# Kernel optimization log

Hardware: AMD Instinct MI355X
Metric: run time of the kernel (lower is better)

## Reference

```python
import jax, jax.numpy as jnp
import numpy as np

M = 4        # multi_anchor
B = 256      # graphs per batch
NPG = 64     # nodes per graph
N = B * NPG  # total nodes
DEG = 8
E = N * DEG
DF = 16      # raw node feature dim
D = 256      # emb_dim
L = 5        # num_layer
NA = 2       # num_anchor
TASKS = 10
T = 1.0


def _gnn_node(h, edge_src, edge_dst, gin_W1, gin_b1, gin_W2, gin_b2, eps):
    # GIN-style message passing: gather -> sum-scatter -> 2-layer MLP, per layer.
    for l in range(L):
        msg = h[:, edge_src]                                  # [M,E,D] gather
        agg = jnp.zeros_like(h).at[:, edge_dst].add(msg)      # [M,N,D] scatter-add
        z = (1.0 + eps[l]) * h + agg
        z = jax.nn.relu(z @ gin_W1[l] + gin_b1[l])
        h = jax.nn.relu(z @ gin_W2[l] + gin_b2[l])
    return h


def _mindist(h):
    # per-node min squared distance to other nodes in the same graph
    hg = h.reshape(M, B, NPG, D)
    sq = jnp.sum(hg * hg, axis=-1)                            # [M,B,n]
    d2 = sq[..., :, None] + sq[..., None, :] - 2.0 * jnp.einsum('mbid,mbjd->mbij', hg, hg)
    d2 = jnp.maximum(d2, 0.0) + jnp.eye(NPG, dtype=h.dtype) * 1e9
    return jnp.min(d2, axis=-1).reshape(M, N)


def reference(x, W_enc, b_enc, gin_W1, gin_b1, gin_W2, gin_b2, eps,
              anchor_emb, W_n2n, b_n2n, W_pred, b_pred, edge_src, edge_dst):
    # InputEncoder (float x -> MLP with tail activation)
    h0 = jax.nn.relu(x @ W_enc + b_enc)                       # [N,D]
    tx = jnp.broadcast_to(h0[None], (M, N, D))                # expand over multi_anchor
    anchor = jnp.zeros((M, N), dtype=jnp.int32)
    xcur = tx
    skey = jax.random.key(42)
    goff = jnp.arange(B) * NPG                                # graph offsets
    rows = jnp.arange(M)[:, None]
    for i in range(1, NA + 1):
        h = _gnn_node(xcur, edge_src, edge_dst, gin_W1, gin_b1, gin_W2, gin_b2, eps)
        mind = _mindist(h)                                    # [M,N]
        pred = -mind - 10.0 * (anchor > 0).astype(h.dtype)    # mask prior anchors
        logits = (pred * T).reshape(M, B, NPG)
        # categorical sample per (anchor-row, graph) via Gumbel-max == multinomial_sample_batch
        u = jax.random.uniform(jax.random.fold_in(skey, i), (M, B, NPG), minval=1e-9, maxval=1.0)
        idx = jnp.argmax(logits - jnp.log(-jnp.log(u)), axis=-1)  # [M,B]
        glob = idx + goff[None, :]
        anchor = anchor.at[rows, glob].set(i)
        xcur = tx * anchor_emb[anchor] + tx
    h = _gnn_node(xcur, edge_src, edge_dst, gin_W1, gin_b1, gin_W2, gin_b2, eps)
    hn = jax.nn.relu(h @ W_n2n + b_n2n)                       # node2node (tailact)
    hg = hn.reshape(M, B, NPG, D).mean(axis=2)                # mean graph pooling
    out = hg @ W_pred + b_pred                                # pred_lin
    return out.mean(axis=0)                                   # mean over multi_anchor -> [B,TASKS]


def setup_inputs():
    key = jax.random.key(0)
    ks = jax.random.split(key, 12)
    x = jax.random.normal(ks[0], (N, DF), dtype=jnp.float32)
    gid = jnp.repeat(jnp.arange(B), NPG * DEG)
    edge_src = gid * NPG + jax.random.randint(ks[1], (E,), 0, NPG)
    edge_dst = gid * NPG + jax.random.randint(ks[2], (E,), 0, NPG)
    s = lambda k, shp: (jax.random.normal(k, shp, dtype=jnp.float32) * 0.05)
    return {
        'x': x,
        'W_enc': s(ks[3], (DF, D)), 'b_enc': jnp.zeros((D,), jnp.float32),
        'gin_W1': s(ks[4], (L, D, D)), 'gin_b1': jnp.zeros((L, D), jnp.float32),
        'gin_W2': s(ks[5], (L, D, D)), 'gin_b2': jnp.zeros((L, D), jnp.float32),
        'eps': jnp.zeros((L,), jnp.float32),
        'anchor_emb': s(ks[6], (NA + 1, D)),
        'W_n2n': s(ks[7], (D, D)), 'b_n2n': jnp.zeros((D,), jnp.float32),
        'W_pred': s(ks[8], (D, TASKS)), 'b_pred': jnp.zeros((TASKS,), jnp.float32),
        'edge_src': edge_src, 'edge_dst': edge_dst,
    }
```

## Files before the change

kernel.cpp:

```cpp
#include <hip/hip_runtime.h>
#include <stdint.h>

typedef unsigned short u16;
typedef _Float16 f16;
typedef f16 f16x8 __attribute__((ext_vector_type(8)));
typedef float f32x16 __attribute__((ext_vector_type(16)));

#define M_     4
#define B_     256
#define NPG_   64
#define N_     (B_*NPG_)
#define DEG_   8
#define E_     (N_*DEG_)
#define DF_    16
#define D_     256
#define L_     5
#define NA_    2
#define TASKS_ 10

#define HROW 520
#define MFMA16(a,b,c) __builtin_amdgcn_mfma_f32_32x32x16_f16(a,b,c,0,0,0)

__device__ __forceinline__ u16 h_bits(f16 h) { union { f16 h; u16 u; } c; c.h = h; return c.u; }
__device__ __forceinline__ f16 bits_h(u16 u) { union { u16 u; f16 h; } c; c.u = u; return c.h; }
__device__ __forceinline__ float h2f(u16 u) { return (float)bits_h(u); }
__device__ __forceinline__ void split_f16(float v, u16& hi, u16& lo) {
  f16 h = (f16)v;
  f16 l = (f16)(v - (float)h);
  hi = h_bits(h); lo = h_bits(l);
}

__device__ __forceinline__ int haddr8(int row, int chunk) {
  return row * HROW + ((chunk ^ (row & 7)) << 4);
}
__device__ __forceinline__ void write_split(u16* hfU, int row, int col, float v) {
  const int ad = haddr8(row, col >> 3) + (col & 7);
  u16 hi, lo; split_f16(v, hi, lo);
  hfU[ad] = hi; hfU[ad + 8] = lo;
}
__device__ __forceinline__ void write_hi(u16* hfU, int row, int col, float v) {
  const int ad = haddr8(row, col >> 3) + (col & 7);
  hfU[ad] = h_bits((f16)v);
}

__device__ __forceinline__ uint32_t rotl32(uint32_t v, int r) { return (v << r) | (v >> (32 - r)); }
__device__ __forceinline__ void threefry2x32(uint32_t k0, uint32_t k1, uint32_t x0, uint32_t x1,
                                             uint32_t& o0, uint32_t& o1) {
  const uint32_t ks2 = k0 ^ k1 ^ 0x1BD11BDAu;
  x0 += k0; x1 += k1;
#define TFR(r) { x0 += x1; x1 = rotl32(x1, r); x1 ^= x0; }
  TFR(13) TFR(15) TFR(26) TFR(6)   x0 += k1;  x1 += ks2 + 1u;
  TFR(17) TFR(29) TFR(16) TFR(24)  x0 += ks2; x1 += k0 + 2u;
  TFR(13) TFR(15) TFR(26) TFR(6)   x0 += k0;  x1 += k1 + 3u;
  TFR(17) TFR(29) TFR(16) TFR(24)  x0 += k1;  x1 += ks2 + 4u;
  TFR(13) TFR(15) TFR(26) TFR(6)   x0 += ks2; x1 += k0 + 5u;
#undef TFR
  o0 = x0; o1 = x1;
}

template<int TERMS>
__device__ __forceinline__ void gemm_w_mfma(u16* __restrict__ hfU, const u16* __restrict__ WTm,
                                            const float* __restrict__ bias, bool do_relu) {
  const int tid = threadIdx.x;
  const int lane = tid & 63, w = tid >> 6;
  const int l31 = lane & 31, lh = lane >> 5;
  const int col = w * 32 + l31;
  const float bv = bias[col];

  f32x16 acc0 = {}, acc1 = {};
  const u16* Bbase = WTm + col * 8;
#pragma unroll
  for (int ks = 0; ks < 16; ++ks) {
    const int chunk = ks * 2 + lh;
    const int a0 = haddr8(l31, chunk);
    const int a1 = haddr8(32 + l31, chunk);
    const f16x8 ahi0 = *(const f16x8*)(hfU + a0);
    const f16x8 ahi1 = *(const f16x8*)(hfU + a1);
    const f16x8 bh = *(const f16x8*)(Bbase + chunk * 2048);
    if (TERMS == 3) {
      const f16x8 alo0 = *(const f16x8*)(hfU + a0 + 8);
      const f16x8 alo1 = *(const f16x8*)(hfU + a1 + 8);
      const f16x8 bl = *(const f16x8*)(Bbase + chunk * 2048 + 65536);
      acc0 = MFMA16(ahi0, bh, acc0);
      acc0 = MFMA16(ahi0, bl, acc0);
      acc0 = MFMA16(alo0, bh, acc0);
      acc1 = MFMA16(ahi1, bh, acc1);
      acc1 = MFMA16(ahi1, bl, acc1);
      acc1 = MFMA16(alo1, bh, acc1);
    } else {
      acc0 = MFMA16(ahi0, bh, acc0);
      acc1 = MFMA16(ahi1, bh, acc1);
    }
  }
  __syncthreads();
#pragma unroll
  for (int r = 0; r < 16; ++r) {
    const int rr = (r & 3) + 8 * (r >> 2) + 4 * lh;
    float v0 = acc0[r] + bv;
    float v1 = acc1[r] + bv;
    if (do_relu) { v0 = fmaxf(v0, 0.f); v1 = fmaxf(v1, 0.f); }
    if (TERMS == 3) {
      write_split(hfU, rr, col, v0);
      write_split(hfU, 32 + rr, col, v1);
    } else {
      write_hi(hfU, rr, col, v0);
      write_hi(hfU, 32 + rr, col, v1);
    }
  }
  __syncthreads();
}

template<int TERMS>
__device__ __forceinline__ void gemm_adj_mfma(u16* __restrict__ hfU, const u16* __restrict__ AdjU,
                                              float epsl) {
  const int tid = threadIdx.x;
  const int lane = tid & 63, w = tid >> 6;
  const int l31 = lane & 31, lh = lane >> 5;
  const int d = w * 32 + l31;
  const int dc = d >> 3, de = d & 7;
  f32x16 acc0 = {}, acc1 = {};
#pragma unroll
  for (int kk = 0; kk < 4; ++kk) {
    const f16x8 A0 = *(const f16x8*)(AdjU + l31 * 72 + (kk * 2 + lh) * 8);
    const f16x8 A1 = *(const f16x8*)(AdjU + (32 + l31) * 72 + (kk * 2 + lh) * 8);
    const int jb = kk * 16 + lh * 8;
    f16x8 bh, bl;
#pragma unroll
    for (int jj = 0; jj < 8; ++jj) {
      const int j = jb + jj;
      const int ad = haddr8(j, dc) + de;
      bh[jj] = bits_h(hfU[ad]);
      if (TERMS == 3) bl[jj] = bits_h(hfU[ad + 8]);
    }
    acc0 = MFMA16(A0, bh, acc0);
    acc1 = MFMA16(A1, bh, acc1);
    if (TERMS == 3) {
      acc0 = MFMA16(A0, bl, acc0);
      acc1 = MFMA16(A1, bl, acc1);
    }
  }
  float self0[16], self1[16];
#pragma unroll
  for (int r = 0; r < 16; ++r) {
    const int rr = (r & 3) + 8 * (r >> 2) + 4 * lh;
    { const int ad = haddr8(rr, dc) + de;
      self0[r] = (TERMS == 3) ? (h2f(hfU[ad]) + h2f(hfU[ad + 8])) : h2f(hfU[ad]); }
    { const int ad = haddr8(32 + rr, dc) + de;
      self1[r] = (TERMS == 3) ? (h2f(hfU[ad]) + h2f(hfU[ad + 8])) : h2f(hfU[ad]); }
  }
  __syncthreads();
#pragma unroll
  for (int r = 0; r < 16; ++r) {
    const int rr = (r & 3) + 8 * (r >> 2) + 4 * lh;
    if (TERMS == 3) {
      write_split(hfU, rr, d, acc0[r] + epsl * self0[r]);
      write_split(hfU, 32 + rr, d, acc1[r] + epsl * self1[r]);
    } else {
      write_hi(hfU, rr, d, acc0[r] + epsl * self0[r]);
      write_hi(hfU, 32 + rr, d, acc1[r] + epsl * self1[r]);
    }
  }
  __syncthreads();
}

__device__ __forceinline__ void mindist_mfma(u16* __restrict__ hfU, float* __restrict__ mindS) {
  const int tid = threadIdx.x;
  const int lane = tid & 63, w = tid >> 6;
  const int gb = w & 3, gi = gb >> 1, gj = gb & 1, ks = w >> 2;
  const int l31 = lane & 31, lh = lane >> 5;
  f32x16 acc = {};
#pragma unroll
  for (int t = 0; t < 8; ++t) {
    const int chunk = 4 * t + 2 * ks + lh;
    const int ra = haddr8(gi * 32 + l31, chunk);
    const int rb_ = haddr8(gj * 32 + l31, chunk);
    const f16x8 ahi = *(const f16x8*)(hfU + ra);
    const f16x8 alo = *(const f16x8*)(hfU + ra + 8);
    const f16x8 bhi = *(const f16x8*)(hfU + rb_);
    const f16x8 blo = *(const f16x8*)(hfU + rb_ + 8);
    acc = MFMA16(ahi, bhi, acc);
    acc = MFMA16(ahi, blo, acc);
    acc = MFMA16(alo, bhi, acc);
  }
  __syncthreads();
  float* hfF = (float*)hfU;
  if (ks == 1) {
#pragma unroll
    for (int r = 0; r < 16; ++r) {
      const int rr = (r & 3) + 8 * (r >> 2) + 4 * lh;
      hfF[gb * 1088 + rr * 34 + l31] = acc[r];
    }
  }
  __syncthreads();
  if (ks == 0) {
#pragma unroll
    for (int r = 0; r < 16; ++r) {
      const int rr = (r & 3) + 8 * (r >> 2) + 4 * lh;
      const float g = acc[r] + hfF[gb * 1088 + rr * 34 + l31];
      hfF[8192 + (gi * 32 + rr) * 66 + gj * 32 + l31] = g;
    }
  }
  __syncthreads();
  {
    const int i = tid >> 3, jt = tid & 7;
    const float gii = hfF[8192 + i * 66 + i];
    float dmin = 3.4e38f;
#pragma unroll
    for (int jj = 0; jj < 8; ++jj) {
      const int j = jt * 8 + jj;
      const float gjj = hfF[8192 + j * 66 + j];
      const float gij = hfF[8192 + i * 66 + j];
      float d2 = fmaxf(gii + gjj - 2.f * gij, 0.f);
      if (j == i) d2 += 1e9f;
      dmin = fminf(dmin, d2);
    }
    dmin = fminf(dmin, __shfl_xor(dmin, 1));
    dmin = fminf(dmin, __shfl_xor(dmin, 2));
    dmin = fminf(dmin, __shfl_xor(dmin, 4));
    if (jt == 0) mindS[i] = dmin;
  }
  __syncthreads();
}

__device__ __forceinline__ void stage_adj(u16* AdjU, const float* AdjF, int b, int tid) {
  const float* src = AdjF + b * 4096;
  for (int t = tid; t < 4096; t += 512)
    AdjU[(t >> 6) * 72 + (t & 63)] = h_bits((f16)src[t]);
}

template<bool WRITE_LO>
__device__ __forceinline__ void build_xcur(u16* hfU, const float* h0g, const float* aemb,
                                           const int* anchorS, int b, int tid) {
  const int i = tid >> 3, part = tid & 7;
  const float* t = h0g + (b * 64 + i) * 256;
  const float* e = aemb + anchorS[i] * D_;
#pragma unroll
  for (int c = 0; c < 4; ++c) {
    const int chunk = part * 4 + c;
    const float4 tv0 = *(const float4*)(t + chunk * 8);
    const float4 tv1 = *(const float4*)(t + chunk * 8 + 4);
    const float4 ev0 = *(const float4*)(e + chunk * 8);
    const float4 ev1 = *(const float4*)(e + chunk * 8 + 4);
    float vv[8];
    vv[0] = fmaf(tv0.x, ev0.x, tv0.x); vv[1] = fmaf(tv0.y, ev0.y, tv0.y);
    vv[2] = fmaf(tv0.z, ev0.z, tv0.z); vv[3] = fmaf(tv0.w, ev0.w, tv0.w);
    vv[4] = fmaf(tv1.x, ev1.x, tv1.x); vv[5] = fmaf(tv1.y, ev1.y, tv1.y);
    vv[6] = fmaf(tv1.z, ev1.z, tv1.z); vv[7] = fmaf(tv1.w, ev1.w, tv1.w);
    f16x8 hi8, lo8;
#pragma unroll
    for (int ee = 0; ee < 8; ++ee) { u16 h, l; split_f16(vv[ee], h, l); hi8[ee] = bits_h(h); lo8[ee] = bits_h(l); }
    const int a = haddr8(i, chunk);
    *(f16x8*)(hfU + a) = hi8;
    if (WRITE_LO) *(f16x8*)(hfU + a + 8) = lo8;
  }
}

__device__ __forceinline__ void sample_anchor(const float* mindS, float* scoreS, int* anchorS,
                                              int m, int b, int iter, int tid) {
  if (tid < 64) {
    const int j = tid;
    uint32_t k0, k1;
    threefry2x32(0u, 42u, 0u, (uint32_t)iter, k0, k1);
    const uint32_t p = (uint32_t)(m * (B_ * NPG_) + b * NPG_ + j);
    uint32_t o0, o1, bits;
    if (p < 32768u) { threefry2x32(k0, k1, p, p + 32768u, o0, o1); bits = o0; }
    else            { threefry2x32(k0, k1, p - 32768u, p, o0, o1); bits = o1; }
    const float f = __uint_as_float((bits >> 9) | 0x3f800000u) - 1.0f;
    const float uv = fmaxf(1e-9f, f + 1e-9f);
    const float pred = -mindS[j] - ((anchorS[j] > 0) ? 10.0f : 0.0f);
    scoreS[j] = pred - logf(-logf(uv));
  }
  __syncthreads();
  if (tid == 0) {
    int best = 0; float bv = scoreS[0];
    for (int j = 1; j < 64; ++j) { const float v = scoreS[j]; if (v > bv) { bv = v; best = j; } }
    anchorS[best] = iter;
  }
}

__global__ void build_adj_kernel(const int* __restrict__ esrc, const int* __restrict__ edst,
                                 float* __restrict__ AdjF) {
  const int e = blockIdx.x * 256 + threadIdx.x;
  if (e < E_) {
    const int s = esrc[e];
    const int d = edst[e];
    const int g = s >> 6;
    atomicAdd(AdjF + g * 4096 + (d & 63) * 64 + (s & 63), 1.0f);
  }
}

__global__ __launch_bounds__(256) void prep_wt(const float* __restrict__ gW1, const float* __restrict__ gW2,
                                               const float* __restrict__ Wn2n, u16* __restrict__ WTbuf) {
  const int mat = blockIdx.x;
  const float* Wsrc = (mat < 5) ? (gW1 + mat * 65536)
                    : (mat < 10) ? (gW2 + (mat - 5) * 65536) : Wn2n;
  u16* dst = WTbuf + (size_t)mat * 131072;
  const int base = blockIdx.y * 2048;
  for (int idx = base + threadIdx.x; idx < base + 2048; idx += 256) {
    const int k = idx >> 8, d = idx & 255;
    const float a = Wsrc[idx];
    u16 hi, lo; split_f16(a, hi, lo);
    const int off = (k >> 3) * 2048 + d * 8 + (k & 7);
    dst[off] = hi;
    dst[65536 + off] = lo;
  }
}

__global__ __launch_bounds__(512)
void gnn1_kernel(const float* __restrict__ x, const float* __restrict__ Wenc,
                 const float* __restrict__ benc, float* __restrict__ h0g,
                 const float* __restrict__ AdjF, const u16* __restrict__ WTbuf,
                 const float* __restrict__ gb1, const float* __restrict__ gb2,
                 const float* __restrict__ eps, float* __restrict__ mindG) {
  __shared__ __align__(16) u16 hfU[64 * HROW];
  __shared__ __align__(16) u16 AdjU[64 * 72];
  __shared__ float mindS[64];
  const int tid = threadIdx.x;
  const int b = blockIdx.x;

  {
    float* scr = (float*)hfU;
    for (int t = tid; t < 4096; t += 512) {
      const int k = t >> 8, d = t & 255;
      scr[k * 264 + d + (d >> 5)] = Wenc[t];
    }
    if (tid < 256) scr[4300 + tid] = benc[tid];
    for (int t = tid; t < 1024; t += 512) scr[4600 + t] = x[b * 1024 + t];
    __syncthreads();

    const int i = tid >> 3, part = tid & 7;
    float xv[16];
#pragma unroll
    for (int k = 0; k < 16; ++k) xv[k] = scr[4600 + i * 16 + k];
    float hv[32];
#pragma unroll
    for (int dd = 0; dd < 32; ++dd) {
      const int d = part * 32 + dd;
      float acc = scr[4300 + d];
#pragma unroll
      for (int k = 0; k < 16; ++k) acc = fmaf(xv[k], scr[k * 264 + d + (d >> 5)], acc);
      hv[dd] = fmaxf(acc, 0.f);
    }
    float* dst = h0g + (b * 64 + i) * 256 + part * 32;
#pragma unroll
    for (int dd = 0; dd < 32; dd += 4) {
      float4 v; v.x = hv[dd]; v.y = hv[dd + 1]; v.z = hv[dd + 2]; v.w = hv[dd + 3];
      *(float4*)(dst + dd) = v;
    }
    __syncthreads();
#pragma unroll
    for (int c = 0; c < 4; ++c) {
      f16x8 hi8, lo8;
#pragma unroll
      for (int e = 0; e < 8; ++e) { u16 h, l; split_f16(hv[c * 8 + e], h, l); hi8[e] = bits_h(h); lo8[e] = bits_h(l); }
      const int a = haddr8(i, part * 4 + c);
      *(f16x8*)(hfU + a) = hi8;
      *(f16x8*)(hfU + a + 8) = lo8;
    }
  }
  stage_adj(AdjU, AdjF, b, tid);
  __syncthreads();

  for (int l = 0; l < L_; ++l) {
    const float epsl = 1.0f + eps[l];
    gemm_adj_mfma<3>(hfU, AdjU, epsl);
    gemm_w_mfma<3>(hfU, WTbuf + (size_t)l * 131072,       gb1 + l * D_, true);
    gemm_w_mfma<3>(hfU, WTbuf + (size_t)(5 + l) * 131072, gb2 + l * D_, true);
  }
  mindist_mfma(hfU, mindS);
  if (tid < 64) mindG[b * 64 + tid] = mindS[tid];
}

__global__ __launch_bounds__(512, 4)
void mega_kernel(const float* __restrict__ h0g, const float* __restrict__ AdjF,
                 const u16* __restrict__ WTbuf,
                 const float* __restrict__ gb1, const float* __restrict__ gb2,
                 const float* __restrict__ eps, const float* __restrict__ aemb,
                 const float* __restrict__ bn2n,
                 const float* __restrict__ Wpred, const float* __restrict__ bpred,
                 const float* __restrict__ mindG, float* __restrict__ outp) {
  __shared__ __align__(16) u16 hfU[64 * HROW];
  __shared__ __align__(16) u16 AdjU[64 * 72];
  __shared__ float mindS[64];
  __shared__ float scoreS[64];
  __shared__ float hgS[256];
  __shared__ int   anchorS[64];

  const int tid = threadIdx.x;
  const int b = blockIdx.x;
  const int m = blockIdx.y;

  stage_adj(AdjU, AdjF, b, tid);
  if (tid < 64) { anchorS[tid] = 0; mindS[tid] = mindG[b * 64 + tid]; }
  __syncthreads();

  sample_anchor(mindS, scoreS, anchorS, m, b, 1, tid);
  __syncthreads();
  build_xcur<true>(hfU, h0g, aemb, anchorS, b, tid);
  __syncthreads();

  for (int l = 0; l < L_; ++l) {
    const float epsl = 1.0f + eps[l];
    gemm_adj_mfma<3>(hfU, AdjU, epsl);
    gemm_w_mfma<3>(hfU, WTbuf + (size_t)l * 131072,       gb1 + l * D_, true);
    gemm_w_mfma<3>(hfU, WTbuf + (size_t)(5 + l) * 131072, gb2 + l * D_, true);
  }
  mindist_mfma(hfU, mindS);
  sample_anchor(mindS, scoreS, anchorS, m, b, 2, tid);
  __syncthreads();
  build_xcur<false>(hfU, h0g, aemb, anchorS, b, tid);
  __syncthreads();

  for (int l = 0; l < L_; ++l) {
    const float epsl = 1.0f + eps[l];
    gemm_adj_mfma<1>(hfU, AdjU, epsl);
    gemm_w_mfma<1>(hfU, WTbuf + (size_t)l * 131072,       gb1 + l * D_, true);
    gemm_w_mfma<1>(hfU, WTbuf + (size_t)(5 + l) * 131072, gb2 + l * D_, true);
  }

  gemm_w_mfma<1>(hfU, WTbuf + (size_t)10 * 131072, bn2n, true);
  if (tid < 256) {
    const int dc = tid >> 3, de = tid & 7;
    float s = 0.f;
    for (int i = 0; i < 64; ++i)
      s += h2f(hfU[haddr8(i, dc) + de]);
    hgS[tid] = s * (1.0f / 64.0f);
  }
  __syncthreads();
  if (tid < 160) {
    const int t = tid >> 4, part = tid & 15;
    float s = 0.f;
    for (int d = part * 16; d < part * 16 + 16; ++d) s = fmaf(hgS[d], Wpred[d * TASKS_ + t], s);
    s += __shfl_xor(s, 1); s += __shfl_xor(s, 2); s += __shfl_xor(s, 4); s += __shfl_xor(s, 8);
    if (part == 0) {
      float val = s * 0.25f;
      if (m == 0) val += bpred[t];
      atomicAdd(outp + b * TASKS_ + t, val);
    }
  }
}

extern "C" void kernel_launch(void* const* d_in, const int* in_sizes, int n_in,
                              void* d_out, int out_size, void* d_ws, size_t ws_size,
                              hipStream_t stream) {
  const float* x     = (const float*)d_in[0];
  const float* Wenc  = (const float*)d_in[1];
  const float* benc  = (const float*)d_in[2];
  const float* gW1   = (const float*)d_in[3];
  const float* gb1   = (const float*)d_in[4];
  const float* gW2   = (const float*)d_in[5];
  const float* gb2   = (const float*)d_in[6];
  const float* eps   = (const float*)d_in[7];
  const float* aemb  = (const float*)d_in[8];
  const float* Wn2n  = (const float*)d_in[9];
  const float* bn2n  = (const float*)d_in[10];
  const float* Wpred = (const float*)d_in[11];
  const float* bpred = (const float*)d_in[12];
  const int* esrc    = (const int*)d_in[13];
  const int* edst    = (const int*)d_in[14];
  float* outp = (float*)d_out;

  float* h0g  = (float*)d_ws;
  float* AdjF = h0g + (size_t)N_ * D_;
  u16* WTbuf  = (u16*)(AdjF + B_ * 4096);
  float* mindG = (float*)(WTbuf + (size_t)11 * 131072);

  hipMemsetAsync(AdjF, 0, (size_t)B_ * 4096 * sizeof(float), stream);
  hipMemsetAsync(outp, 0, (size_t)out_size * sizeof(float), stream);
  build_adj_kernel<<<dim3((E_ + 255) / 256), dim3(256), 0, stream>>>(esrc, edst, AdjF);
  prep_wt<<<dim3(11, 32), dim3(256), 0, stream>>>(gW1, gW2, Wn2n, WTbuf);
  gnn1_kernel<<<dim3(B_), dim3(512), 0, stream>>>(x, Wenc, benc, h0g, AdjF, WTbuf,
                                                  gb1, gb2, eps, mindG);
  mega_kernel<<<dim3(B_, M_), dim3(512), 0, stream>>>(h0g, AdjF, WTbuf, gb1, gb2,
                                                      eps, aemb, bn2n, Wpred, bpred, mindG, outp);
}
```

Before: 673.4 us.

## Split-K 1024-thread first GNN pass and ping-pong buffers in light GNN

The first-iteration GNN kernel (one block per graph, only 256 blocks) moves to 1024 threads, and its weight GEMMs are split along K across two wave groups with an LDS reduction. This raises per-block parallelism on a grid too small to fill the GPU. The low-precision second pass now ping-pongs between the hi and lo halves of the shared buffer, which lets each stage drop one barrier between reading and writing. Costs are extra LDS reduction traffic and barriers in the split-K path, plus idle waves in the adjacency and mindist stages.

After: 699.8 us. 1.04x slower.

```diff
diff --git a/kernel.cpp b/kernel.cpp
--- a/kernel.cpp
+++ b/kernel.cpp
@@ -37,10 +37,6 @@
   const int ad = haddr8(row, col >> 3) + (col & 7);
   u16 hi, lo; split_f16(v, hi, lo);
   hfU[ad] = hi; hfU[ad + 8] = lo;
-}
-__device__ __forceinline__ void write_hi(u16* hfU, int row, int col, float v) {
-  const int ad = haddr8(row, col >> 3) + (col & 7);
-  hfU[ad] = h_bits((f16)v);
 }
 
 __device__ __forceinline__ uint32_t rotl32(uint32_t v, int r) { return (v << r) | (v >> (32 - r)); }
@@ -58,8 +54,7 @@
   o0 = x0; o1 = x1;
 }
 
-template<int TERMS>
-__device__ __forceinline__ void gemm_w_mfma(u16* __restrict__ hfU, const u16* __restrict__ WTm,
+__device__ __forceinline__ void gemm_w_full(u16* __restrict__ hfU, const u16* __restrict__ WTm,
                                             const float* __restrict__ bias, bool do_relu) {
   const int tid = threadIdx.x;
   const int lane = tid & 63, w = tid >> 6;
@@ -76,21 +71,16 @@
     const int a1 = haddr8(32 + l31, chunk);
     const f16x8 ahi0 = *(const f16x8*)(hfU + a0);
     const f16x8 ahi1 = *(const f16x8*)(hfU + a1);
+    const f16x8 alo0 = *(const f16x8*)(hfU + a0 + 8);
+    const f16x8 alo1 = *(const f16x8*)(hfU + a1 + 8);
     const f16x8 bh = *(const f16x8*)(Bbase + chunk * 2048);
-    if (TERMS == 3) {
-      const f16x8 alo0 = *(const f16x8*)(hfU + a0 + 8);
-      const f16x8 alo1 = *(const f16x8*)(hfU + a1 + 8);
-      const f16x8 bl = *(const f16x8*)(Bbase + chunk * 2048 + 65536);
-      acc0 = MFMA16(ahi0, bh, acc0);
-      acc0 = MFMA16(ahi0, bl, acc0);
-      acc0 = MFMA16(alo0, bh, acc0);
-      acc1 = MFMA16(ahi1, bh, acc1);
-      acc1 = MFMA16(ahi1, bl, acc1);
-      acc1 = MFMA16(alo1, bh, acc1);
-    } else {
-      acc0 = MFMA16(ahi0, bh, acc0);
-      acc1 = MFMA16(ahi1, bh, acc1);
-    }
+    const f16x8 bl = *(const f16x8*)(Bbase + chunk * 2048 + 65536);
+    acc0 = MFMA16(ahi0, bh, acc0);
+    acc0 = MFMA16(ahi0, bl, acc0);
+    acc0 = MFMA16(alo0, bh, acc0);
+    acc1 = MFMA16(ahi1, bh, acc1);
+    acc1 = MFMA16(ahi1, bl, acc1);
+    acc1 = MFMA16(alo1, bh, acc1);
   }
   __syncthreads();
 #pragma unroll
@@ -99,19 +89,13 @@
     float v0 = acc0[r] + bv;
     float v1 = acc1[r] + bv;
     if (do_relu) { v0 = fmaxf(v0, 0.f); v1 = fmaxf(v1, 0.f); }
-    if (TERMS == 3) {
-      write_split(hfU, rr, col, v0);
-      write_split(hfU, 32 + rr, col, v1);
-    } else {
-      write_hi(hfU, rr, col, v0);
-      write_hi(hfU, 32 + rr, col, v1);
-    }
-  }
-  __syncthreads();
-}
-
-template<int TERMS>
-__device__ __forceinline__ void gemm_adj_mfma(u16* __restrict__ hfU, const u16* __restrict__ AdjU,
+    write_split(hfU, rr, col, v0);
+    write_split(hfU, 32 + rr, col, v1);
+  }
+  __syncthreads();
+}
+
+__device__ __forceinline__ void gemm_adj_full(u16* __restrict__ hfU, const u16* __restrict__ AdjU,
                                               float epsl) {
   const int tid = threadIdx.x;
   const int lane = tid & 63, w = tid >> 6;
@@ -127,38 +111,28 @@
     f16x8 bh, bl;
 #pragma unroll
     for (int jj = 0; jj < 8; ++jj) {
-      const int j = jb + jj;
-      const int ad = haddr8(j, dc) + de;
+      const int ad = haddr8(jb + jj, dc) + de;
       bh[jj] = bits_h(hfU[ad]);
-      if (TERMS == 3) bl[jj] = bits_h(hfU[ad + 8]);
+      bl[jj] = bits_h(hfU[ad + 8]);
     }
     acc0 = MFMA16(A0, bh, acc0);
     acc1 = MFMA16(A1, bh, acc1);
-    if (TERMS == 3) {
-      acc0 = MFMA16(A0, bl, acc0);
-      acc1 = MFMA16(A1, bl, acc1);
-    }
+    acc0 = MFMA16(A0, bl, acc0);
+    acc1 = MFMA16(A1, bl, acc1);
   }
   float self0[16], self1[16];
 #pragma unroll
   for (int r = 0; r < 16; ++r) {
     const int rr = (r & 3) + 8 * (r >> 2) + 4 * lh;
-    { const int ad = haddr8(rr, dc) + de;
-      self0[r] = (TERMS == 3) ? (h2f(hfU[ad]) + h2f(hfU[ad + 8])) : h2f(hfU[ad]); }
-    { const int ad = haddr8(32 + rr, dc) + de;
-      self1[r] = (TERMS == 3) ? (h2f(hfU[ad]) + h2f(hfU[ad + 8])) : h2f(hfU[ad]); }
+    { const int ad = haddr8(rr, dc) + de;      self0[r] = h2f(hfU[ad]) + h2f(hfU[ad + 8]); }
+    { const int ad = haddr8(32 + rr, dc) + de; self1[r] = h2f(hfU[ad]) + h2f(hfU[ad + 8]); }
   }
   __syncthreads();
 #pragma unroll
   for (int r = 0; r < 16; ++r) {
     const int rr = (r & 3) + 8 * (r >> 2) + 4 * lh;
-    if (TERMS == 3) {
-      write_split(hfU, rr, d, acc0[r] + epsl * self0[r]);
-      write_split(hfU, 32 + rr, d, acc1[r] + epsl * self1[r]);
-    } else {
-      write_hi(hfU, rr, d, acc0[r] + epsl * self0[r]);
-      write_hi(hfU, 32 + rr, d, acc1[r] + epsl * self1[r]);
-    }
+    write_split(hfU, rr, d, acc0[r] + epsl * self0[r]);
+    write_split(hfU, 32 + rr, d, acc1[r] + epsl * self1[r]);
   }
   __syncthreads();
 }
@@ -222,9 +196,244 @@
   __syncthreads();
 }
 
-__device__ __forceinline__ void stage_adj(u16* AdjU, const float* AdjF, int b, int tid) {
+__device__ __forceinline__ void gemm_w_light(u16* __restrict__ hfU, const u16* __restrict__ WTm,
+                                             const float* __restrict__ bias, bool do_relu,
+                                             int pin, int pout) {
+  const int tid = threadIdx.x;
+  const int lane = tid & 63, w = tid >> 6;
+  const int l31 = lane & 31, lh = lane >> 5;
+  const int col = w * 32 + l31;
+  const float bv = bias[col];
+  f32x16 acc0 = {}, acc1 = {};
+  const u16* Bbase = WTm + col * 8;
+#pragma unroll
+  for (int ks = 0; ks < 16; ++ks) {
+    const int chunk = ks * 2 + lh;
+    const f16x8 a0 = *(const f16x8*)(hfU + haddr8(l31, chunk) + pin);
+    const f16x8 a1 = *(const f16x8*)(hfU + haddr8(32 + l31, chunk) + pin);
+    const f16x8 bh = *(const f16x8*)(Bbase + chunk * 2048);
+    acc0 = MFMA16(a0, bh, acc0);
+    acc1 = MFMA16(a1, bh, acc1);
+  }
+#pragma unroll
+  for (int r = 0; r < 16; ++r) {
+    const int rr = (r & 3) + 8 * (r >> 2) + 4 * lh;
+    float v0 = acc0[r] + bv, v1 = acc1[r] + bv;
+    if (do_relu) { v0 = fmaxf(v0, 0.f); v1 = fmaxf(v1, 0.f); }
+    hfU[haddr8(rr, col >> 3) + (col & 7) + pout] = h_bits((f16)v0);
+    hfU[haddr8(32 + rr, col >> 3) + (col & 7) + pout] = h_bits((f16)v1);
+  }
+  __syncthreads();
+}
+
+__device__ __forceinline__ void gemm_adj_light(u16* __restrict__ hfU, const u16* __restrict__ AdjU,
+                                               float epsl, int pin, int pout) {
+  const int tid = threadIdx.x;
+  const int lane = tid & 63, w = tid >> 6;
+  const int l31 = lane & 31, lh = lane >> 5;
+  const int d = w * 32 + l31;
+  const int dc = d >> 3, de = d & 7;
+  f32x16 acc0 = {}, acc1 = {};
+#pragma unroll
+  for (int kk = 0; kk < 4; ++kk) {
+    const f16x8 A0 = *(const f16x8*)(AdjU + l31 * 72 + (kk * 2 + lh) * 8);
+    const f16x8 A1 = *(const f16x8*)(AdjU + (32 + l31) * 72 + (kk * 2 + lh) * 8);
+    const int jb = kk * 16 + lh * 8;
+    f16x8 bh;
+#pragma unroll
+    for (int jj = 0; jj < 8; ++jj)
+      bh[jj] = bits_h(hfU[haddr8(jb + jj, dc) + de + pin]);
+    acc0 = MFMA16(A0, bh, acc0);
+    acc1 = MFMA16(A1, bh, acc1);
+  }
+#pragma unroll
+  for (int r = 0; r < 16; ++r) {
+    const int rr = (r & 3) + 8 * (r >> 2) + 4 * lh;
+    const float s0 = h2f(hfU[haddr8(rr, dc) + de + pin]);
+    const float s1 = h2f(hfU[haddr8(32 + rr, dc) + de + pin]);
+    hfU[haddr8(rr, dc) + de + pout]      = h_bits((f16)(acc0[r] + epsl * s0));
+    hfU[haddr8(32 + rr, dc) + de + pout] = h_bits((f16)(acc1[r] + epsl * s1));
+  }
+  __syncthreads();
+}
+
+__device__ __forceinline__ void gemm_w3_ks1024(u16* __restrict__ hfU, const u16* __restrict__ WTm,
+                                               const float* __restrict__ bias, bool do_relu) {
+  const int tid = threadIdx.x;
+  const int lane = tid & 63, w = tid >> 6;
+  const int l31 = lane & 31, lh = lane >> 5;
+  const int ks = w >> 3;
+  const int cb = w & 7;
+  const int col = cb * 32 + l31;
+  const float bv = bias[col];
+
+  f32x16 acc0 = {}, acc1 = {};
+  const u16* Bbase = WTm + col * 8;
+#pragma unroll
+  for (int q = 0; q < 8; ++q) {
+    const int chunk = ks * 16 + q * 2 + lh;
+    const int a0 = haddr8(l31, chunk);
+    const int a1 = haddr8(32 + l31, chunk);
+    const f16x8 ahi0 = *(const f16x8*)(hfU + a0);
+    const f16x8 ahi1 = *(const f16x8*)(hfU + a1);
+    const f16x8 alo0 = *(const f16x8*)(hfU + a0 + 8);
+    const f16x8 alo1 = *(const f16x8*)(hfU + a1 + 8);
+    const f16x8 bh = *(const f16x8*)(Bbase + chunk * 2048);
+    const f16x8 bl = *(const f16x8*)(Bbase + chunk * 2048 + 65536);
+    acc0 = MFMA16(ahi0, bh, acc0);
+    acc0 = MFMA16(ahi0, bl, acc0);
+    acc0 = MFMA16(alo0, bh, acc0);
+    acc1 = MFMA16(ahi1, bh, acc1);
+    acc1 = MFMA16(ahi1, bl, acc1);
+    acc1 = MFMA16(alo1, bh, acc1);
+  }
+  __syncthreads();
+  float* scr = (float*)hfU;
+  if (ks == 1) {
+#pragma unroll
+    for (int r = 0; r < 16; ++r) {
+      const int rr = (r & 3) + 8 * (r >> 2) + 4 * lh;
+      scr[(cb * 64 + rr) * 32 + l31]      = acc0[r];
+      scr[(cb * 64 + 32 + rr) * 32 + l31] = acc1[r];
+    }
+  }
+  __syncthreads();
+  float sc0[16], sc1[16];
+  if (ks == 0) {
+#pragma unroll
+    for (int r = 0; r < 16; ++r) {
+      const int rr = (r & 3) + 8 * (r >> 2) + 4 * lh;
+      sc0[r] = scr[(cb * 64 + rr) * 32 + l31];
+      sc1[r] = scr[(cb * 64 + 32 + rr) * 32 + l31];
+    }
+  }
+  __syncthreads();
+  if (ks == 0) {
+#pragma unroll
+    for (int r = 0; r < 16; ++r) {
+      const int rr = (r & 3) + 8 * (r >> 2) + 4 * lh;
+      float v0 = acc0[r] + sc0[r] + bv;
+      float v1 = acc1[r] + sc1[r] + bv;
+      if (do_relu) { v0 = fmaxf(v0, 0.f); v1 = fmaxf(v1, 0.f); }
+      write_split(hfU, rr, col, v0);
+      write_split(hfU, 32 + rr, col, v1);
+    }
+  }
+  __syncthreads();
+}
+
+__device__ __forceinline__ void gemm_adj3_1024(u16* __restrict__ hfU, const u16* __restrict__ AdjU,
+                                               float epsl) {
+  const int tid = threadIdx.x;
+  const int lane = tid & 63, w = tid >> 6;
+  const int l31 = lane & 31, lh = lane >> 5;
+  const bool act = (w < 8);
+  const int d = (w & 7) * 32 + l31;
+  const int dc = d >> 3, de = d & 7;
+  f32x16 acc0 = {}, acc1 = {};
+  float self0[16], self1[16];
+  if (act) {
+#pragma unroll
+    for (int kk = 0; kk < 4; ++kk) {
+      const f16x8 A0 = *(const f16x8*)(AdjU + l31 * 72 + (kk * 2 + lh) * 8);
+      const f16x8 A1 = *(const f16x8*)(AdjU + (32 + l31) * 72 + (kk * 2 + lh) * 8);
+      const int jb = kk * 16 + lh * 8;
+      f16x8 bh, bl;
+#pragma unroll
+      for (int jj = 0; jj < 8; ++jj) {
+        const int ad = haddr8(jb + jj, dc) + de;
+        bh[jj] = bits_h(hfU[ad]);
+        bl[jj] = bits_h(hfU[ad + 8]);
+      }
+      acc0 = MFMA16(A0, bh, acc0);
+      acc1 = MFMA16(A1, bh, acc1);
+      acc0 = MFMA16(A0, bl, acc0);
+      acc1 = MFMA16(A1, bl, acc1);
+    }
+#pragma unroll
+    for (int r = 0; r < 16; ++r) {
+      const int rr = (r & 3) + 8 * (r >> 2) + 4 * lh;
+      { const int ad = haddr8(rr, dc) + de;      self0[r] = h2f(hfU[ad]) + h2f(hfU[ad + 8]); }
+      { const int ad = haddr8(32 + rr, dc) + de; self1[r] = h2f(hfU[ad]) + h2f(hfU[ad + 8]); }
+    }
+  }
+  __syncthreads();
+  if (act) {
+#pragma unroll
+    for (int r = 0; r < 16; ++r) {
+      const int rr = (r & 3) + 8 * (r >> 2) + 4 * lh;
+      write_split(hfU, rr, d, acc0[r] + epsl * self0[r]);
+      write_split(hfU, 32 + rr, d, acc1[r] + epsl * self1[r]);
+    }
+  }
+  __syncthreads();
+}
+
+__device__ __forceinline__ void mindist_1024(u16* __restrict__ hfU, float* __restrict__ mindS) {
+  const int tid = threadIdx.x;
+  const int lane = tid & 63, w = tid >> 6;
+  const bool act = (w < 8);
+  const int gb = w & 3, gi = gb >> 1, gj = gb & 1, ks = (w >> 2) & 1;
+  const int l31 = lane & 31, lh = lane >> 5;
+  f32x16 acc = {};
+  if (act) {
+#pragma unroll
+    for (int t = 0; t < 8; ++t) {
+      const int chunk = 4 * t + 2 * ks + lh;
+      const int ra = haddr8(gi * 32 + l31, chunk);
+      const int rb_ = haddr8(gj * 32 + l31, chunk);
+      const f16x8 ahi = *(const f16x8*)(hfU + ra);
+      const f16x8 alo = *(const f16x8*)(hfU + ra + 8);
+      const f16x8 bhi = *(const f16x8*)(hfU + rb_);
+      const f16x8 blo = *(const f16x8*)(hfU + rb_ + 8);
+      acc = MFMA16(ahi, bhi, acc);
+      acc = MFMA16(ahi, blo, acc);
+      acc = MFMA16(alo, bhi, acc);
+    }
+  }
+  __syncthreads();
+  float* hfF = (float*)hfU;
+  if (act && ks == 1) {
+#pragma unroll
+    for (int r = 0; r < 16; ++r) {
+      const int rr = (r & 3) + 8 * (r >> 2) + 4 * lh;
+      hfF[gb * 1088 + rr * 34 + l31] = acc[r];
+    }
+  }
+  __syncthreads();
+  if (act && ks == 0) {
+#pragma unroll
+    for (int r = 0; r < 16; ++r) {
+      const int rr = (r & 3) + 8 * (r >> 2) + 4 * lh;
+      const float g = acc[r] + hfF[gb * 1088 + rr * 34 + l31];
+      hfF[8192 + (gi * 32 + rr) * 66 + gj * 32 + l31] = g;
+    }
+  }
+  __syncthreads();
+  if (tid < 512) {
+    const int i = tid >> 3, jt = tid & 7;
+    const float gii = hfF[8192 + i * 66 + i];
+    float dmin = 3.4e38f;
+#pragma unroll
+    for (int jj = 0; jj < 8; ++jj) {
+      const int j = jt * 8 + jj;
+      const float gjj = hfF[8192 + j * 66 + j];
+      const float gij = hfF[8192 + i * 66 + j];
+      float d2 = fmaxf(gii + gjj - 2.f * gij, 0.f);
+      if (j == i) d2 += 1e9f;
+      dmin = fminf(dmin, d2);
+    }
+    dmin = fminf(dmin, __shfl_xor(dmin, 1));
+    dmin = fminf(dmin, __shfl_xor(dmin, 2));
+    dmin = fminf(dmin, __shfl_xor(dmin, 4));
+    if (jt == 0) mindS[i] = dmin;
+  }
+  __syncthreads();
+}
+
+__device__ __forceinline__ void stage_adj(u16* AdjU, const float* AdjF, int b, int tid, int T) {
   const float* src = AdjF + b * 4096;
-  for (int t = tid; t < 4096; t += 512)
+  for (int t = tid; t < 4096; t += T)
     AdjU[(t >> 6) * 72 + (t & 63)] = h_bits((f16)src[t]);
 }
 
@@ -306,7 +515,7 @@
   }
 }
 
-__global__ __launch_bounds__(512)
+__global__ __launch_bounds__(1024)
 void gnn1_kernel(const float* __restrict__ x, const float* __restrict__ Wenc,
                  const float* __restrict__ benc, float* __restrict__ h0g,
                  const float* __restrict__ AdjF, const u16* __restrict__ WTbuf,
@@ -320,54 +529,54 @@
 
   {
     float* scr = (float*)hfU;
-    for (int t = tid; t < 4096; t += 512) {
+    for (int t = tid; t < 4096; t += 1024) {
       const int k = t >> 8, d = t & 255;
       scr[k * 264 + d + (d >> 5)] = Wenc[t];
     }
     if (tid < 256) scr[4300 + tid] = benc[tid];
-    for (int t = tid; t < 1024; t += 512) scr[4600 + t] = x[b * 1024 + t];
+    if (tid < 1024) scr[4600 + tid] = x[b * 1024 + tid];
     __syncthreads();
 
-    const int i = tid >> 3, part = tid & 7;
+    const int i = tid >> 4, part = tid & 15;
     float xv[16];
 #pragma unroll
     for (int k = 0; k < 16; ++k) xv[k] = scr[4600 + i * 16 + k];
-    float hv[32];
-#pragma unroll
-    for (int dd = 0; dd < 32; ++dd) {
-      const int d = part * 32 + dd;
+    float hv[16];
+#pragma unroll
+    for (int dd = 0; dd < 16; ++dd) {
+      const int d = part * 16 + dd;
       float acc = scr[4300 + d];
 #pragma unroll
       for (int k = 0; k < 16; ++k) acc = fmaf(xv[k], scr[k * 264 + d + (d >> 5)], acc);
       hv[dd] = fmaxf(acc, 0.f);
     }
-    float* dst = h0g + (b * 64 + i) * 256 + part * 32;
-#pragma unroll
-    for (int dd = 0; dd < 32; dd += 4) {
+    float* dst = h0g + (b * 64 + i) * 256 + part * 16;
+#pragma unroll
+    for (int dd = 0; dd < 16; dd += 4) {
       float4 v; v.x = hv[dd]; v.y = hv[dd + 1]; v.z = hv[dd + 2]; v.w = hv[dd + 3];
       *(float4*)(dst + dd) = v;
     }
     __syncthreads();
 #pragma unroll
-    for (int c = 0; c < 4; ++c) {
+    for (int c = 0; c < 2; ++c) {
       f16x8 hi8, lo8;
 #pragma unroll
       for (int e = 0; e < 8; ++e) { u16 h, l; split_f16(hv[c * 8 + e], h, l); hi8[e] = bits_h(h); lo8[e] = bits_h(l); }
-      const int a = haddr8(i, part * 4 + c);
+      const int a = haddr8(i, part * 2 + c);
       *(f16x8*)(hfU + a) = hi8;
       *(f16x8*)(hfU + a + 8) = lo8;
     }
   }
-  stage_adj(AdjU, AdjF, b, tid);
+  stage_adj(AdjU, AdjF, b, tid, 1024);
   __syncthreads();
 
   for (int l = 0; l < L_; ++l) {
     const float epsl = 1.0f + eps[l];
-    gemm_adj_mfma<3>(hfU, AdjU, epsl);
-    gemm_w_mfma<3>(hfU, WTbuf + (size_t)l * 131072,       gb1 + l * D_, true);
-    gemm_w_mfma<3>(hfU, WTbuf + (size_t)(5 + l) * 131072, gb2 + l * D_, true);
-  }
-  mindist_mfma(hfU, mindS);
+    gemm_adj3_1024(hfU, AdjU, epsl);
+    gemm_w3_ks1024(hfU, WTbuf + (size_t)l * 131072,       gb1 + l * D_, true);
+    gemm_w3_ks1024(hfU, WTbuf + (size_t)(5 + l) * 131072, gb2 + l * D_, true);
+  }
+  mindist_1024(hfU, mindS);
   if (tid < 64) mindG[b * 64 + tid] = mindS[tid];
 }
 
@@ -390,7 +599,7 @@
   const int b = blockIdx.x;
   const int m = blockIdx.y;
 
-  stage_adj(AdjU, AdjF, b, tid);
+  stage_adj(AdjU, AdjF, b, tid, 512);
   if (tid < 64) { anchorS[tid] = 0; mindS[tid] = mindG[b * 64 + tid]; }
   __syncthreads();
 
@@ -401,9 +610,9 @@
 
   for (int l = 0; l < L_; ++l) {
     const float epsl = 1.0f + eps[l];
-    gemm_adj_mfma<3>(hfU, AdjU, epsl);
-    gemm_w_mfma<3>(hfU, WTbuf + (size_t)l * 131072,       gb1 + l * D_, true);
-    gemm_w_mfma<3>(hfU, WTbuf + (size_t)(5 + l) * 131072, gb2 + l * D_, true);
+    gemm_adj_full(hfU, AdjU, epsl);
+    gemm_w_full(hfU, WTbuf + (size_t)l * 131072,       gb1 + l * D_, true);
+    gemm_w_full(hfU, WTbuf + (size_t)(5 + l) * 131072, gb2 + l * D_, true);
   }
   mindist_mfma(hfU, mindS);
   sample_anchor(mindS, scoreS, anchorS, m, b, 2, tid);
@@ -411,14 +620,15 @@
   build_xcur<false>(hfU, h0g, aemb, anchorS, b, tid);
   __syncthreads();
 
+  int p = 0;
   for (int l = 0; l < L_; ++l) {
     const float epsl = 1.0f + eps[l];
-    gemm_adj_mfma<1>(hfU, AdjU, epsl);
-    gemm_w_mfma<1>(hfU, WTbuf + (size_t)l * 131072,       gb1 + l * D_, true);
-    gemm_w_mfma<1>(hfU, WTbuf + (size_t)(5 + l) * 131072, gb2 + l * D_, true);
-  }
-
-  gemm_w_mfma<1>(hfU, WTbuf + (size_t)10 * 131072, bn2n, true);
+    gemm_adj_light(hfU, AdjU, epsl, p, 8 - p); p = 8 - p;
+    gemm_w_light(hfU, WTbuf + (size_t)l * 131072,       gb1 + l * D_, true, p, 8 - p); p = 8 - p;
+    gemm_w_light(hfU, WTbuf + (size_t)(5 + l) * 131072, gb2 + l * D_, true, p, 8 - p); p = 8 - p;
+  }
+  gemm_w_light(hfU, WTbuf + (size_t)10 * 131072, bn2n, true, p, 8 - p); p = 8 - p;
+
   if (tid < 256) {
     const int dc = tid >> 3, de = tid & 7;
     float s = 0.f;
@@ -469,8 +679,8 @@
   hipMemsetAsync(outp, 0, (size_t)out_size * sizeof(float), stream);
   build_adj_kernel<<<dim3((E_ + 255) / 256), dim3(256), 0, stream>>>(esrc, edst, AdjF);
   prep_wt<<<dim3(11, 32), dim3(256), 0, stream>>>(gW1, gW2, Wn2n, WTbuf);
-  gnn1_kernel<<<dim3(B_), dim3(512), 0, stream>>>(x, Wenc, benc, h0g, AdjF, WTbuf,
-                                                  gb1, gb2, eps, mindG);
+  gnn1_kernel<<<dim3(B_), dim3(1024), 0, stream>>>(x, Wenc, benc, h0g, AdjF, WTbuf,
+                                                   gb1, gb2, eps, mindG);
   mega_kernel<<<dim3(B_, M_), dim3(512), 0, stream>>>(h0g, AdjF, WTbuf, gb1, gb2,
                                                       eps, aemb, bn2n, Wpred, bpred, mindG, outp);
 }
```
